# Kernel tuning notes

Hardware: AMD Instinct MI355X
Metric: run time of the kernel (lower is better)

The kernel has to match this reference:

```python
import jax, jax.numpy as jnp
import numpy as np

B, N, IN_DIM, HID, K = 32, 512, 1024, 512, 3
ALPHA = 0.2  # leaky_relu negative slope
NEG = -9e15


def setup_inputs() -> dict:
    key = jax.random.key(0)
    ks = jax.random.split(key, 7)
    hidden_states = jax.random.normal(ks[0], (B, N, IN_DIM), jnp.float32)
    adj = (jax.random.uniform(ks[1], (B, 3, N, N)) < 0.05).astype(jnp.float32)
    W_all = jax.random.normal(ks[2], (3, K, IN_DIM, HID), jnp.float32) * 0.02
    a_all = jax.random.normal(ks[3], (3, K, 2 * HID, 1), jnp.float32) * 0.02
    wawa_w = jax.random.normal(ks[4], (HID, 100), jnp.float32) * 0.05
    wawa_b = jnp.zeros((100,), jnp.float32)
    ctx_w = jax.random.normal(ks[5], (100, 1), jnp.float32) * 0.05
    return {"hidden_states": hidden_states, "adj": adj, "W_all": W_all,
            "a_all": a_all, "wawa_w": wawa_w, "wawa_b": wawa_b, "ctx_w": ctx_w}


def _gat(adj_m, x, W, a):
    # e_ij = leaky_relu(cat[h_i, h_j] @ a) == leaky_relu(h_i@a1 + h_j@a2)
    h = jnp.einsum('bnf,fh->bnh', x, W)           # [B,N,HID]
    f1 = jnp.einsum('bnh,ho->bno', h, a[:HID])    # [B,N,1]
    f2 = jnp.einsum('bnh,ho->bno', h, a[HID:])    # [B,N,1]
    e = jax.nn.leaky_relu(f1 + jnp.swapaxes(f2, 1, 2), negative_slope=ALPHA)  # [B,N,N]
    att = jnp.where(adj_m > 0, e, NEG)
    att = jax.nn.softmax(att, axis=2)
    return jnp.einsum('bnm,bmh->bnh', att, h)


def reference(hidden_states, adj, W_all, a_all, wawa_w, wawa_b, ctx_w):
    adj_a, adj_b, adj_c = adj[:, 0], adj[:, 1], adj[:, 2]
    pa, pb, pc = adj_a, adj_b, adj_c  # matmuls(A, k) = A^(k+1)
    hs = []
    for layer in range(K):
        if layer > 0:
            pa = jnp.matmul(pa, adj_a)
            pb = jnp.matmul(pb, adj_b)
            pc = jnp.matmul(pc, adj_c)
        h_layer = (_gat(pa, hidden_states, W_all[0, layer], a_all[0, layer])
                   + _gat(pb, hidden_states, W_all[1, layer], a_all[1, layer])
                   + _gat(pc, hidden_states, W_all[2, layer], a_all[2, layer]))
        hs.append(h_layer)
    # attention-based combination over the K orders
    s = [jnp.einsum('bnc,co->bno', jnp.tanh(jnp.einsum('bnh,hc->bnc', h, wawa_w) + wawa_b), ctx_w)
         for h in hs]                              # each [B,N,1]
    vs = jax.nn.softmax(jnp.concatenate(s, axis=2), axis=2)  # [B,N,K]
    h_stack = jnp.stack(hs, axis=2)                # [B,N,K,HID]
    return jnp.sum(vs[..., None] * h_stack, axis=2)  # [B,N,HID]
```

## Files before the change

kernel.cpp:

```cpp
#include <hip/hip_runtime.h>
#include <hip/hip_bf16.h>

typedef short v8s __attribute__((ext_vector_type(8)));
typedef float v4f __attribute__((ext_vector_type(4)));
typedef unsigned long long u64;

#define ALPHA 0.2f

__device__ inline unsigned short f32_bf16(float x){
    unsigned int u = __float_as_uint(x);
    unsigned int r = (u + 0x7fffu + ((u >> 16) & 1u)) >> 16;
    return (unsigned short)r;
}
__device__ inline float bf16_f32(unsigned short s){
    return __uint_as_float(((unsigned int)s) << 16);
}
__device__ inline v4f mfma16(v8s a, v8s b, v4f c){
    return __builtin_amdgcn_mfma_f32_16x16x32_bf16(a, b, c, 0, 0, 0);
}
__device__ inline void gload16(const unsigned short* g, short* l){
    __builtin_amdgcn_global_load_lds((const __attribute__((address_space(1))) unsigned int*)g,
                                     (__attribute__((address_space(3))) unsigned int*)l,
                                     16, 0, 0);
}


__global__ void k_convert_x(const float* __restrict__ x, v8s* __restrict__ out, int n8){
    int i = blockIdx.x * 256 + threadIdx.x;
    if (i >= n8) return;
    const float4* p = (const float4*)x + (size_t)i * 2;
    float4 a = p[0], b = p[1];
    v8s r;
    r[0] = (short)f32_bf16(a.x); r[1] = (short)f32_bf16(a.y);
    r[2] = (short)f32_bf16(a.z); r[3] = (short)f32_bf16(a.w);
    r[4] = (short)f32_bf16(b.x); r[5] = (short)f32_bf16(b.y);
    r[6] = (short)f32_bf16(b.z); r[7] = (short)f32_bf16(b.w);
    out[i] = r;
}

__global__ void k_transpose_w(const float* __restrict__ W, unsigned short* __restrict__ Wt){
    __shared__ float tile[32][33];
    int g = blockIdx.z, k0 = blockIdx.x * 32, h0 = blockIdx.y * 32;
    int tx = threadIdx.x, ty = threadIdx.y;
    #pragma unroll
    for (int i = 0; i < 4; ++i)
        tile[ty + i*8][tx] = W[((size_t)g*1024 + k0 + ty + i*8)*512 + h0 + tx];
    __syncthreads();
    #pragma unroll
    for (int i = 0; i < 4; ++i){
        int h = ty + i*8;
        Wt[((size_t)g*512 + h0 + h)*1024 + k0 + tx] = f32_bf16(tile[tx][h]);
    }
}

__global__ void k_wawat(const float* __restrict__ w, unsigned short* __restrict__ wt){
    int i = blockIdx.x * 256 + threadIdx.x;
    if (i >= 128 * 512) return;
    int c = i >> 9, k = i & 511;
    wt[i] = (c < 100) ? f32_bf16(w[k*100 + c]) : (unsigned short)0;
}


__global__ __launch_bounds__(256) void k_bits(const float* __restrict__ adj,
                                              u64* __restrict__ bits){
    int row = blockIdx.x * 4 + (threadIdx.x >> 6);
    int t = row >> 14, b = (row >> 9) & 31, i = row & 511;
    const float* src = adj + (((size_t)b*3 + t)*512 + i)*512;
    int lane = threadIdx.x & 63;
    #pragma unroll
    for (int w = 0; w < 8; ++w){
        u64 word = __ballot(src[w*64 + lane] > 0.5f);
        if (lane == 0) bits[(size_t)row*8 + w] = word;
    }
}

__global__ __launch_bounds__(256) void k_boolmm(const u64* __restrict__ prev,
                                                const u64* __restrict__ base,
                                                u64* __restrict__ out){
    int row = blockIdx.x * 256 + threadIdx.x;
    if (row >= 49152) return;
    int tb = row >> 9;
    const u64* pr = prev + (size_t)row * 8;
    const u64* bb = base + ((size_t)tb << 9) * 8;
    ulonglong2 a0 = {0,0}, a1 = {0,0}, a2 = {0,0}, a3 = {0,0};
    #pragma unroll
    for (int w = 0; w < 8; ++w){
        u64 m = pr[w];
        const u64* bw = bb + (size_t)(w << 6) * 8;
        while (m){
            int k = __builtin_ctzll(m);
            m &= m - 1;
            const ulonglong2* br = (const ulonglong2*)(bw + (size_t)k * 8);
            ulonglong2 b0 = br[0], b1 = br[1], b2 = br[2], b3 = br[3];
            a0.x |= b0.x; a0.y |= b0.y;
            a1.x |= b1.x; a1.y |= b1.y;
            a2.x |= b2.x; a2.y |= b2.y;
            a3.x |= b3.x; a3.y |= b3.y;
        }
    }
    ulonglong2* op = (ulonglong2*)(out + (size_t)row * 8);
    op[0] = a0; op[1] = a1; op[2] = a2; op[3] = a3;
}

__global__ __launch_bounds__(256, 4) void k_gemm_h(
    const unsigned short* __restrict__ Wt, const unsigned short* __restrict__ Xb,
    unsigned short* __restrict__ Ht, const float* __restrict__ aall,
    float* __restrict__ f1p, float* __restrict__ f2p, int l)
{
    __shared__ __align__(16) short As[128*32];
    __shared__ __align__(16) short Bs[128*32];
    const int bn = blockIdx.x, bm = blockIdx.y, t = blockIdx.z;
    const int g = t*3 + l;
    const int tid = threadIdx.x;
    const int lane = tid & 63, wave = tid >> 6;
    const int wr = wave >> 1, wc = wave & 1;
    const int fr = lane & 15, fq = lane >> 4;
    const int slot = fq ^ (fr & 3) ^ ((fr >> 2) & 3);

    const int srow = tid >> 2, sw = tid & 3;
    const int gw = sw ^ (srow & 3) ^ ((srow >> 2) & 3);
    const unsigned short* Ap = Wt + ((size_t)g*512 + (size_t)bm*128 + srow)*1024 + gw*8;
    const unsigned short* Bp = Xb + ((size_t)bn*128 + srow)*1024 + gw*8;
    short* AsW = As + wave*512;
    short* BsW = Bs + wave*512;

    v4f acc[4][4] = {};

    for (int kt = 0; kt < 32; ++kt){
        const unsigned short* a0 = Ap + kt*32;
        const unsigned short* b0 = Bp + kt*32;
        gload16(a0,           AsW);
        gload16(a0 + 64*1024, AsW + 2048);
        gload16(b0,           BsW);
        gload16(b0 + 64*1024, BsW + 2048);
        __syncthreads();
        v8s af[4], bf[4];
        #pragma unroll
        for (int i = 0; i < 4; ++i) af[i] = *(const v8s*)&As[(wr*64 + i*16 + fr)*32 + slot*8];
        #pragma unroll
        for (int i = 0; i < 4; ++i) bf[i] = *(const v8s*)&Bs[(wc*64 + i*16 + fr)*32 + slot*8];
        #pragma unroll
        for (int i = 0; i < 4; ++i)
            #pragma unroll
            for (int j = 0; j < 4; ++j)
                acc[i][j] = mfma16(af[i], bf[j], acc[i][j]);
        __syncthreads();
    }
    #pragma unroll
    for (int i = 0; i < 4; ++i){
        const int h = bm*128 + wr*64 + i*16 + fq*4;
        #pragma unroll
        for (int j = 0; j < 4; ++j){
            const int mc = bn*128 + wc*64 + j*16 + fr;
            unsigned short* dst = Ht + ((size_t)t*512 + h)*16384 + mc;
            #pragma unroll
            for (int rg = 0; rg < 4; ++rg)
                dst[(size_t)rg*16384] = f32_bf16(acc[i][j][rg]);
        }
    }
    const float* a1 = aall + ((size_t)t*3 + l)*1024;
    const float* a2 = a1 + 512;
    float s1[4] = {0.f,0.f,0.f,0.f}, s2[4] = {0.f,0.f,0.f,0.f};
    #pragma unroll
    for (int i = 0; i < 4; ++i){
        #pragma unroll
        for (int rg = 0; rg < 4; ++rg){
            const int h = bm*128 + wr*64 + i*16 + fq*4 + rg;
            const float c1 = a1[h], c2 = a2[h];
            #pragma unroll
            for (int j = 0; j < 4; ++j){
                s1[j] += acc[i][j][rg]*c1;
                s2[j] += acc[i][j][rg]*c2;
            }
        }
    }
    #pragma unroll
    for (int j = 0; j < 4; ++j){
        s1[j] += __shfl_xor(s1[j], 16); s1[j] += __shfl_xor(s1[j], 32);
        s2[j] += __shfl_xor(s2[j], 16); s2[j] += __shfl_xor(s2[j], 32);
    }
    float* scr = (float*)As;
    __syncthreads();
    if (fq == 0){
        #pragma unroll
        for (int j = 0; j < 4; ++j){
            scr[(((wr*2 + wc)*4 + j)*16 + fr)*2 + 0] = s1[j];
            scr[(((wr*2 + wc)*4 + j)*16 + fr)*2 + 1] = s2[j];
        }
    }
    __syncthreads();
    if (tid < 256){
        const int which = tid & 1, fr2 = (tid >> 1) & 15, j2 = (tid >> 5) & 3,
                  wc2 = (tid >> 7) & 1;
        const float v = scr[(((0*2 + wc2)*4 + j2)*16 + fr2)*2 + which]
                      + scr[(((1*2 + wc2)*4 + j2)*16 + fr2)*2 + which];
        const int m = bn*128 + wc2*64 + j2*16 + fr2;
        float* dst = which ? f2p : f1p;
        dst[((size_t)bm*3 + t)*16384 + m] = v;
    }
}

__global__ __launch_bounds__(256) void k_f1red(
    const float* __restrict__ f1p, const float* __restrict__ f2p,
    float* __restrict__ f1, float* __restrict__ f2)
{
    int idx = blockIdx.x * 256 + threadIdx.x;
    if (idx >= 49152) return;
    float s1 = 0.f, s2 = 0.f;
    #pragma unroll
    for (int bm = 0; bm < 4; ++bm){
        int t = idx >> 14, m = idx & 16383;
        s1 += f1p[((size_t)bm*3 + t)*16384 + m];
        s2 += f2p[((size_t)bm*3 + t)*16384 + m];
    }
    f1[idx] = s1; f2[idx] = s2;
}

__device__ inline void softmax_row(int t, int b, int rt, int r, int q,
    const float* __restrict__ f1a, const float* __restrict__ f2a,
    const u64* __restrict__ maskP, float* p)
{
    const float f1v = f1a[t*16384 + b*512 + rt*64 + r];
    const u64 mw = maskP[(((size_t)t*32 + b)*512 + rt*64 + r)*8 + q];
    const float4* f2p = (const float4*)(f2a + t*16384 + b*512 + q*64);
    float sm = 0.f;
    #pragma unroll
    for (int w = 0; w < 16; ++w){
        float4 f4 = f2p[w];
        #pragma unroll
        for (int u2 = 0; u2 < 4; ++u2){
            int u = w*4 + u2;
            float e = f1v + ((const float*)&f4)[u2];
            e = (e >= 0.f) ? e : ALPHA*e;
            float pe = ((mw >> u) & 1ull) ? __expf(e) : 0.f;
            p[u] = pe; sm += pe;
        }
    }
    sm += __shfl_xor(sm, 1);
    sm += __shfl_xor(sm, 2);
    sm += __shfl_xor(sm, 4);
    const float rinv = 1.f / (sm + 1e-30f);
    #pragma unroll
    for (int u = 0; u < 64; ++u) p[u] *= rinv;
}

__device__ inline void store_att(short* __restrict__ attbuf, int r, int q,
                                 const float* p)
{
    #pragma unroll
    for (int j8 = 0; j8 < 8; ++j8){
        v8s pk;
        #pragma unroll
        for (int u = 0; u < 8; ++u) pk[u] = (short)f32_bf16(p[j8*8 + u]);
        const int cs = q*8 + (j8 ^ q);
        *(v8s*)&attbuf[r*520 + cs*8] = pk;
    }
}

__device__ inline void pv_accum(const short* __restrict__ attbuf,
    const unsigned short* __restrict__ Hb, int wave, int fr, int fq, v4f acc[4][4])
{
    v8s bv0[4], bv1[4];
    #pragma unroll
    for (int j = 0; j < 4; ++j)
        bv0[j] = *(const v8s*)(Hb + (size_t)(wave*64 + j*16 + fr)*16384 + fq*8);
    #pragma unroll
    for (int kk = 0; kk < 16; ++kk){
        if (kk + 1 < 16){
            if ((kk + 1) & 1){
                #pragma unroll
                for (int j = 0; j < 4; ++j)
                    bv1[j] = *(const v8s*)(Hb + (size_t)(wave*64 + j*16 + fr)*16384
                                           + (kk+1)*32 + fq*8);
            } else {
                #pragma unroll
                for (int j = 0; j < 4; ++j)
                    bv0[j] = *(const v8s*)(Hb + (size_t)(wave*64 + j*16 + fr)*16384
                                           + (kk+1)*32 + fq*8);
            }
        }
        v8s af[4];
        const int cb = kk*4 + fq;
        const int cs = (cb & 56) | ((cb & 7) ^ ((cb >> 3) & 7));
        #pragma unroll
        for (int i = 0; i < 4; ++i)
            af[i] = *(const v8s*)&attbuf[(i*16 + fr)*520 + cs*8];
        if (kk & 1){
            #pragma unroll
            for (int i = 0; i < 4; ++i)
                #pragma unroll
                for (int j = 0; j < 4; ++j)
                    acc[i][j] = mfma16(af[i], bv1[j], acc[i][j]);
        } else {
            #pragma unroll
            for (int i = 0; i < 4; ++i)
                #pragma unroll
                for (int j = 0; j < 4; ++j)
                    acc[i][j] = mfma16(af[i], bv0[j], acc[i][j]);
        }
    }
}

__global__ __launch_bounds__(512, 2) void k_att_pv(
    const unsigned short* __restrict__ Ht,
    const float* __restrict__ f1a, const float* __restrict__ f2a,
    const u64* __restrict__ maskP,
    unsigned short* __restrict__ hlb)
{
    __shared__ __align__(16) short att0[64*520];
    __shared__ __align__(16) short att1[64*520];
    const int tid = threadIdx.x;
    const int lane = tid & 63, wave = tid >> 6;
    const int b = blockIdx.x, rt = blockIdx.y;
    const int r = tid >> 3, q = tid & 7;
    const int fr = lane & 15, fq = lane >> 4;
    v4f acc[4][4] = {};
    float p[64];

    const unsigned short* Hb0 = Ht + (size_t)b*512;

    softmax_row(0, b, rt, r, q, f1a, f2a, maskP, p);
    store_att(att0, r, q, p);
    __syncthreads();

    softmax_row(1, b, rt, r, q, f1a, f2a, maskP, p);
    store_att(att1, r, q, p);
    pv_accum(att0, Hb0, wave, fr, fq, acc);
    __syncthreads();

    softmax_row(2, b, rt, r, q, f1a, f2a, maskP, p);
    store_att(att0, r, q, p);
    pv_accum(att1, Hb0 + (size_t)512*16384, wave, fr, fq, acc);
    __syncthreads();

    pv_accum(att0, Hb0 + (size_t)2*512*16384, wave, fr, fq, acc);

    #pragma unroll
    for (int i = 0; i < 4; ++i){
        const int row = rt*64 + i*16 + fq*4;
        #pragma unroll
        for (int j = 0; j < 4; ++j){
            const int col = wave*64 + j*16 + fr;
            unsigned short* d1 = hlb + ((size_t)b*512 + row)*512 + col;
            #pragma unroll
            for (int rg = 0; rg < 4; ++rg)
                d1[(size_t)rg*512] = f32_bf16(acc[i][j][rg]);
        }
    }
}

__global__ __launch_bounds__(256) void k_gemm_s(
    const unsigned short* __restrict__ Hb, const unsigned short* __restrict__ Wwt,
    float* __restrict__ C1)
{
    __shared__ __align__(16) short As[128*32];
    __shared__ __align__(16) short Bs[128*32];
    const int bm = blockIdx.x;
    const int tid = threadIdx.x;
    const int lane = tid & 63, wave = tid >> 6;
    const int wr = wave >> 1, wc = wave & 1;
    const int fr = lane & 15, fq = lane >> 4;
    const int slot = fq ^ (fr & 3) ^ ((fr >> 2) & 3);
    const int srow = tid >> 2, sw = tid & 3;
    const int gw = sw ^ (srow & 3) ^ ((srow >> 2) & 3);
    const unsigned short* Ap = Hb + ((size_t)bm*128 + srow)*512 + gw*8;
    const unsigned short* Bp = Wwt + (size_t)srow*512 + gw*8;

    v4f acc[4][4] = {};
    v8s ra0 = *(const v8s*)(Ap);
    v8s ra1 = *(const v8s*)(Ap + 64*512);
    v8s rb0 = *(const v8s*)(Bp);
    v8s rb1 = *(const v8s*)(Bp + 64*512);

    for (int kt = 0; kt < 16; ++kt){
        __syncthreads();
        *(v8s*)&As[tid*8]        = ra0;
        *(v8s*)&As[tid*8 + 2048] = ra1;
        *(v8s*)&Bs[tid*8]        = rb0;
        *(v8s*)&Bs[tid*8 + 2048] = rb1;
        __syncthreads();
        if (kt + 1 < 16){
            const unsigned short* An = Ap + (kt+1)*32;
            const unsigned short* Bn = Bp + (kt+1)*32;
            ra0 = *(const v8s*)(An); ra1 = *(const v8s*)(An + 64*512);
            rb0 = *(const v8s*)(Bn); rb1 = *(const v8s*)(Bn + 64*512);
        }
        v8s af[4], bf[4];
        #pragma unroll
        for (int i = 0; i < 4; ++i) af[i] = *(const v8s*)&As[(wr*64 + i*16 + fr)*32 + slot*8];
        #pragma unroll
        for (int i = 0; i < 4; ++i) bf[i] = *(const v8s*)&Bs[(wc*64 + i*16 + fr)*32 + slot*8];
        #pragma unroll
        for (int i = 0; i < 4; ++i)
            #pragma unroll
            for (int j = 0; j < 4; ++j)
                acc[i][j] = mfma16(af[i], bf[j], acc[i][j]);
    }
    #pragma unroll
    for (int i = 0; i < 4; ++i)
        #pragma unroll
        for (int j = 0; j < 4; ++j)
            #pragma unroll
            for (int rg = 0; rg < 4; ++rg)
                C1[((size_t)bm*128 + wr*64 + i*16 + fq*4 + rg)*128 + wc*64 + j*16 + fr]
                    = acc[i][j][rg];
}

__global__ void k_sv(const float* __restrict__ C1, const float* __restrict__ wb,
                     const float* __restrict__ cw, float* __restrict__ v)
{
    int m = blockIdx.x * 256 + threadIdx.x;
    if (m >= 16384) return;
    float s[3];
    #pragma unroll
    for (int l = 0; l < 3; ++l){
        const float* row = C1 + ((size_t)l*16384 + m)*128;
        float a = 0.f;
        for (int c = 0; c < 100; ++c){
            float x = row[c] + wb[c];
            float th;
            if (x > 15.f) th = 1.f;
            else if (x < -15.f) th = -1.f;
            else { float ex = __expf(2.f*x); th = (ex - 1.f) / (ex + 1.f); }
            a += th * cw[c];
        }
        s[l] = a;
    }
    float m0 = fmaxf(s[0], fmaxf(s[1], s[2]));
    float e0 = __expf(s[0]-m0), e1 = __expf(s[1]-m0), e2 = __expf(s[2]-m0);
    float inv = 1.f / (e0 + e1 + e2);
    v[m] = e0*inv; v[16384 + m] = e1*inv; v[32768 + m] = e2*inv;
}

__global__ void k_comb(const unsigned short* __restrict__ hlb, const float* __restrict__ v,
                       float* __restrict__ out)
{
    int idx = blockIdx.x * 256 + threadIdx.x;
    if (idx >= 16384*64) return;
    int m = idx >> 6, c8 = (idx & 63) << 3;
    const unsigned short* hp = hlb + (size_t)m*512 + c8;
    v8s a = *(const v8s*)hp;
    v8s bb = *(const v8s*)(hp + (size_t)16384*512);
    v8s cc = *(const v8s*)(hp + (size_t)2*16384*512);
    float v0 = v[m], v1 = v[16384+m], v2 = v[32768+m];
    float o[8];
    #pragma unroll
    for (int u = 0; u < 8; ++u)
        o[u] = v0*bf16_f32((unsigned short)a[u])
             + v1*bf16_f32((unsigned short)bb[u])
             + v2*bf16_f32((unsigned short)cc[u]);
    float4* dst = (float4*)(out + (size_t)m*512 + c8);
    dst[0] = make_float4(o[0], o[1], o[2], o[3]);
    dst[1] = make_float4(o[4], o[5], o[6], o[7]);
}

extern "C" void kernel_launch(void* const* d_in, const int* in_sizes, int n_in,
                              void* d_out, int out_size, void* d_ws, size_t ws_size,
                              hipStream_t stream)
{
    (void)in_sizes; (void)n_in; (void)out_size; (void)ws_size;
    const float* hs   = (const float*)d_in[0];
    const float* adj  = (const float*)d_in[1];
    const float* W    = (const float*)d_in[2];
    const float* aall = (const float*)d_in[3];
    const float* ww   = (const float*)d_in[4];
    const float* wb   = (const float*)d_in[5];
    const float* cw   = (const float*)d_in[6];
    float* out = (float*)d_out;
    char* ws = (char*)d_ws;

    unsigned short* Xb  = (unsigned short*)(ws);
    unsigned short* Wt  = (unsigned short*)(ws + 33554432);
    unsigned short* Wwt = (unsigned short*)(ws + 42991616);
    u64* bits           = (u64*)(ws + 43122688);
    u64* P2             = (u64*)(ws + 46268416);
    u64* P3             = (u64*)(ws + 49414144);
    unsigned short* Ht  = (unsigned short*)(ws + 52559872);
    float* f1           = (float*)(ws + 102891520);
    float* f2           = (float*)(ws + 103088128);
    float* f1p          = (float*)(ws + 103284736);
    float* f2p          = (float*)(ws + 104071168);
    unsigned short* hlb = (unsigned short*)(ws + 203948032);
    float* C1           = (float*)(ws + 52559872);
    float* vv           = (float*)(ws + 102891520);

    k_convert_x<<<8192, 256, 0, stream>>>(hs, (v8s*)Xb, 2097152);
    k_transpose_w<<<dim3(32,16,9), dim3(32,8), 0, stream>>>(W, Wt);
    k_wawat<<<256, 256, 0, stream>>>(ww, Wwt);
    k_bits<<<12288, 256, 0, stream>>>(adj, bits);
    k_boolmm<<<192, 256, 0, stream>>>(bits, bits, P2);
    k_boolmm<<<192, 256, 0, stream>>>(bits, P2, P3);

    const u64* masks[3] = {bits, P2, P3};
    for (int l = 0; l < 3; ++l){
        k_gemm_h<<<dim3(128,4,3), 256, 0, stream>>>(Wt, Xb, Ht, aall, f1p, f2p, l);
        k_f1red<<<192, 256, 0, stream>>>(f1p, f2p, f1, f2);
        k_att_pv<<<dim3(32,8), 512, 0, stream>>>(Ht, f1, f2, masks[l],
            hlb + (size_t)l*16384*512);
    }
    k_gemm_s<<<384, 256, 0, stream>>>(hlb, Wwt, C1);
    k_sv<<<64, 256, 0, stream>>>(C1, wb, cw, vv);
    k_comb<<<4096, 256, 0, stream>>>(hlb, vv, out);
}
```

Baseline: 592.9 us.

## Deepen PV global-load prefetch and transpose C1 for coalesced score reads

```diff
diff --git a/kernel.cpp b/kernel.cpp
--- a/kernel.cpp
+++ b/kernel.cpp
@@ -257,49 +257,39 @@
     }
 }
 
-__device__ inline void pv_accum(const short* __restrict__ attbuf,
-    const unsigned short* __restrict__ Hb, int wave, int fr, int fq, v4f acc[4][4])
-{
-    v8s bv0[4], bv1[4];
-    #pragma unroll
-    for (int j = 0; j < 4; ++j)
-        bv0[j] = *(const v8s*)(Hb + (size_t)(wave*64 + j*16 + fr)*16384 + fq*8);
-    #pragma unroll
-    for (int kk = 0; kk < 16; ++kk){
-        if (kk + 1 < 16){
-            if ((kk + 1) & 1){
-                #pragma unroll
-                for (int j = 0; j < 4; ++j)
-                    bv1[j] = *(const v8s*)(Hb + (size_t)(wave*64 + j*16 + fr)*16384
-                                           + (kk+1)*32 + fq*8);
-            } else {
-                #pragma unroll
-                for (int j = 0; j < 4; ++j)
-                    bv0[j] = *(const v8s*)(Hb + (size_t)(wave*64 + j*16 + fr)*16384
-                                           + (kk+1)*32 + fq*8);
-            }
-        }
-        v8s af[4];
-        const int cb = kk*4 + fq;
-        const int cs = (cb & 56) | ((cb & 7) ^ ((cb >> 3) & 7));
-        #pragma unroll
-        for (int i = 0; i < 4; ++i)
-            af[i] = *(const v8s*)&attbuf[(i*16 + fr)*520 + cs*8];
-        if (kk & 1){
-            #pragma unroll
-            for (int i = 0; i < 4; ++i)
-                #pragma unroll
-                for (int j = 0; j < 4; ++j)
-                    acc[i][j] = mfma16(af[i], bv1[j], acc[i][j]);
-        } else {
-            #pragma unroll
-            for (int i = 0; i < 4; ++i)
-                #pragma unroll
-                for (int j = 0; j < 4; ++j)
-                    acc[i][j] = mfma16(af[i], bv0[j], acc[i][j]);
-        }
-    }
-}
+#define PV_LOAD(buf, kknum) { \
+    _Pragma("unroll") \
+    for (int j = 0; j < 4; ++j) \
+        buf[j] = *(const v8s*)(Hb + (size_t)(wave*64 + j*16 + fr)*16384 + (kknum)*32 + fq*8); }
+
+#define PV_MFMA(buf) { \
+    _Pragma("unroll") \
+    for (int i = 0; i < 4; ++i) \
+        _Pragma("unroll") \
+        for (int j = 0; j < 4; ++j) \
+            acc[i][j] = mfma16(af[i], buf[j], acc[i][j]); }
+
+#define PV_BODY(ATT) { \
+    _Pragma("unroll") \
+    for (int kk = 0; kk < 16; ++kk){ \
+        const int nx = kk + 3; \
+        if (nx < 16){ \
+            if (nx % 4 == 0)      { PV_LOAD(bva, nx) } \
+            else if (nx % 4 == 1) { PV_LOAD(bvb, nx) } \
+            else if (nx % 4 == 2) { PV_LOAD(bvc, nx) } \
+            else                  { PV_LOAD(bvd, nx) } \
+        } \
+        v8s af[4]; \
+        const int cb = kk*4 + fq; \
+        const int cs = (cb & 56) | ((cb & 7) ^ ((cb >> 3) & 7)); \
+        _Pragma("unroll") \
+        for (int i = 0; i < 4; ++i) \
+            af[i] = *(const v8s*)&ATT[(i*16 + fr)*520 + cs*8]; \
+        if (kk % 4 == 0)      { PV_MFMA(bva) } \
+        else if (kk % 4 == 1) { PV_MFMA(bvb) } \
+        else if (kk % 4 == 2) { PV_MFMA(bvc) } \
+        else                  { PV_MFMA(bvd) } \
+    } }
 
 __global__ __launch_bounds__(512, 2) void k_att_pv(
     const unsigned short* __restrict__ Ht,
@@ -316,24 +306,30 @@
     const int fr = lane & 15, fq = lane >> 4;
     v4f acc[4][4] = {};
     float p[64];
-
-    const unsigned short* Hb0 = Ht + (size_t)b*512;
-
+    v8s bva[4], bvb[4], bvc[4], bvd[4];
+
+    const unsigned short* Hb = Ht + (size_t)b*512;
+
+    PV_LOAD(bva, 0); PV_LOAD(bvb, 1); PV_LOAD(bvc, 2);
     softmax_row(0, b, rt, r, q, f1a, f2a, maskP, p);
     store_att(att0, r, q, p);
     __syncthreads();
 
     softmax_row(1, b, rt, r, q, f1a, f2a, maskP, p);
     store_att(att1, r, q, p);
-    pv_accum(att0, Hb0, wave, fr, fq, acc);
+    PV_BODY(att0);
     __syncthreads();
 
+    Hb += (size_t)512*16384;
+    PV_LOAD(bva, 0); PV_LOAD(bvb, 1); PV_LOAD(bvc, 2);
     softmax_row(2, b, rt, r, q, f1a, f2a, maskP, p);
     store_att(att0, r, q, p);
-    pv_accum(att1, Hb0 + (size_t)512*16384, wave, fr, fq, acc);
+    PV_BODY(att1);
     __syncthreads();
 
-    pv_accum(att0, Hb0 + (size_t)2*512*16384, wave, fr, fq, acc);
+    Hb += (size_t)512*16384;
+    PV_LOAD(bva, 0); PV_LOAD(bvb, 1); PV_LOAD(bvc, 2);
+    PV_BODY(att0);
 
     #pragma unroll
     for (int i = 0; i < 4; ++i){
@@ -351,7 +347,7 @@
 
 __global__ __launch_bounds__(256) void k_gemm_s(
     const unsigned short* __restrict__ Hb, const unsigned short* __restrict__ Wwt,
-    float* __restrict__ C1)
+    float* __restrict__ C1t)
 {
     __shared__ __align__(16) short As[128*32];
     __shared__ __align__(16) short Bs[128*32];
@@ -397,16 +393,17 @@
                 acc[i][j] = mfma16(af[i], bf[j], acc[i][j]);
     }
     #pragma unroll
-    for (int i = 0; i < 4; ++i)
-        #pragma unroll
-        for (int j = 0; j < 4; ++j)
-            #pragma unroll
-            for (int rg = 0; rg < 4; ++rg)
-                C1[((size_t)bm*128 + wr*64 + i*16 + fq*4 + rg)*128 + wc*64 + j*16 + fr]
-                    = acc[i][j][rg];
-}
-
-__global__ void k_sv(const float* __restrict__ C1, const float* __restrict__ wb,
+    for (int i = 0; i < 4; ++i){
+        const int m0 = bm*128 + wr*64 + i*16 + fq*4;
+        #pragma unroll
+        for (int j = 0; j < 4; ++j){
+            const int c = wc*64 + j*16 + fr;
+            *(v4f*)&C1t[(size_t)c*49152 + m0] = acc[i][j];
+        }
+    }
+}
+
+__global__ void k_sv(const float* __restrict__ C1t, const float* __restrict__ wb,
                      const float* __restrict__ cw, float* __restrict__ v)
 {
     int m = blockIdx.x * 256 + threadIdx.x;
@@ -414,10 +411,10 @@
     float s[3];
     #pragma unroll
     for (int l = 0; l < 3; ++l){
-        const float* row = C1 + ((size_t)l*16384 + m)*128;
+        const float* col = C1t + l*16384 + m;
         float a = 0.f;
         for (int c = 0; c < 100; ++c){
-            float x = row[c] + wb[c];
+            float x = col[(size_t)c*49152] + wb[c];
             float th;
             if (x > 15.f) th = 1.f;
             else if (x < -15.f) th = -1.f;
@@ -481,7 +478,7 @@
     float* f1p          = (float*)(ws + 103284736);
     float* f2p          = (float*)(ws + 104071168);
     unsigned short* hlb = (unsigned short*)(ws + 203948032);
-    float* C1           = (float*)(ws + 52559872);
+    float* C1t          = (float*)(ws + 52559872);
     float* vv           = (float*)(ws + 102891520);
 
     k_convert_x<<<8192, 256, 0, stream>>>(hs, (v8s*)Xb, 2097152);
@@ -498,7 +495,7 @@
         k_att_pv<<<dim3(32,8), 512, 0, stream>>>(Ht, f1, f2, masks[l],
             hlb + (size_t)l*16384*512);
     }
-    k_gemm_s<<<384, 256, 0, stream>>>(hlb, Wwt, C1);
-    k_sv<<<64, 256, 0, stream>>>(C1, wb, cw, vv);
+    k_gemm_s<<<384, 256, 0, stream>>>(hlb, Wwt, C1t);
+    k_sv<<<64, 256, 0, stream>>>(C1t, wb, cw, vv);
     k_comb<<<4096, 256, 0, stream>>>(hlb, vv, out);
 }
```

Measured after the change: 642.9 us. 8.4% more time.
